# Performance work log

Measured on AMD Instinct MI355X. Metric: run time of the kernel, lower is better.

Reference implementation:

```python
import jax, jax.numpy as jnp
import numpy as np

N_SRC = 100000
N_DST = 50000
N_EDGES = 800000
D = 128
D_OUT = 128


def setup_inputs() -> dict:
    key = jax.random.key(0)
    ks = jax.random.split(key, 8)
    H_src = jax.random.normal(ks[0], (N_SRC, D), dtype=jnp.float32)
    H_dst = jax.random.normal(ks[1], (N_DST, D), dtype=jnp.float32)
    HBar_src = jax.random.normal(ks[2], (N_SRC, D), dtype=jnp.float32)
    agg_HBar_dst = jax.random.normal(ks[3], (N_DST, D), dtype=jnp.float32)
    src_idx = jax.random.randint(ks[4], (N_EDGES,), 0, N_SRC, dtype=jnp.int64)
    dst_idx = jax.random.randint(ks[5], (N_EDGES,), 0, N_DST, dtype=jnp.int64)
    # Linear(in_feats*2, out_feats): store as [2D, D_OUT] for x @ W + b
    gain = float(np.sqrt(2.0))  # calculate_gain('relu')
    bound = gain * float(np.sqrt(6.0 / (2 * D + D_OUT)))  # xavier_uniform
    W = jax.random.uniform(ks[6], (2 * D, D_OUT), dtype=jnp.float32,
                           minval=-bound, maxval=bound)
    b = jnp.zeros((D_OUT,), dtype=jnp.float32)
    return {"H_src": H_src, "H_dst": H_dst, "HBar_src": HBar_src,
            "agg_HBar_dst": agg_HBar_dst, "W": W, "b": b,
            "src_idx": src_idx, "dst_idx": dst_idx}


def reference(H_src, H_dst, HBar_src, agg_HBar_dst, W, b, src_idx, dst_idx):
    # training path of SAGEConvWithCV: copy_u('hdelta') + mean over dst
    hdelta = H_src - HBar_src                      # [N_src, D]
    msgs = jnp.take(hdelta, src_idx, axis=0)       # [E, D] gather
    summed = jax.ops.segment_sum(msgs, dst_idx, num_segments=N_DST)  # [N_dst, D]
    deg = jax.ops.segment_sum(jnp.ones((src_idx.shape[0],), dtype=H_src.dtype),
                              dst_idx, num_segments=N_DST)           # [N_dst]
    hdelta_new = summed / jnp.maximum(deg, 1.0)[:, None]  # mean (0 for isolated)
    h_neigh = agg_HBar_dst + hdelta_new
    h = jnp.concatenate([H_dst, h_neigh], axis=1) @ W + b  # [N_dst, D_OUT]
    return jax.nn.relu(h)
```

## Files before the change

kernel.cpp:

```cpp
#include <hip/hip_runtime.h>
#include <hip/hip_bf16.h>
#include <cstdint>
#include <cstddef>

#define NSRC 100000
#define NDST 50000
#define DOUT 128
#define KK2 256
#define NBUCK 196
#define CHUNK 4096

typedef __attribute__((ext_vector_type(8))) short bf16x8;
typedef __attribute__((ext_vector_type(4))) float f32x4;
typedef __attribute__((ext_vector_type(2))) float f32x2;

static __device__ __forceinline__ unsigned short f2bf(float f) {
    union { float f; uint32_t u; } v; v.f = f;
    uint32_t u = v.u;
    uint32_t r = u + 0x7FFFu + ((u >> 16) & 1u);
    return (unsigned short)(r >> 16);
}

__global__ __launch_bounds__(256) void k_prep(const float* __restrict__ W,
                                              unsigned short* __restrict__ WT,
                                              int* __restrict__ bcnt) {
    int i = blockIdx.x * 256 + threadIdx.x;
    if (i < DOUT * KK2) {
        int n = i >> 8;
        int k = i & 255;
        WT[i] = f2bf(W[k * DOUT + n]);
    }
    if (i < 256) bcnt[i] = 0;
}

__global__ __launch_bounds__(256) void k_hdelta(const float4* __restrict__ a,
                                                const float4* __restrict__ b,
                                                uint2* __restrict__ o, int n8) {
    int i = blockIdx.x * 256 + threadIdx.x;
    if (i < n8) {
        float4 x0 = a[i * 2],     y0 = b[i * 2];
        float4 x1 = a[i * 2 + 1], y1 = b[i * 2 + 1];
        uint32_t p0 = __builtin_amdgcn_cvt_pk_fp8_f32(x0.x - y0.x, x0.y - y0.y, 0u, false);
        p0 = __builtin_amdgcn_cvt_pk_fp8_f32(x0.z - y0.z, x0.w - y0.w, p0, true);
        uint32_t p1 = __builtin_amdgcn_cvt_pk_fp8_f32(x1.x - y1.x, x1.y - y1.y, 0u, false);
        p1 = __builtin_amdgcn_cvt_pk_fp8_f32(x1.z - y1.z, x1.w - y1.w, p1, true);
        o[i] = make_uint2(p0, p1);
    }
}

__global__ __launch_bounds__(256) void k_binA1(const int* __restrict__ dst,
                                               int* __restrict__ bcnt, int E) {
    __shared__ int bh[NBUCK];
    int t = threadIdx.x;
    if (t < NBUCK) bh[t] = 0;
    __syncthreads();
    int base = blockIdx.x * CHUNK;
    for (int i = t; i < CHUNK; i += 256) {
        int e = base + i;
        if (e < E) atomicAdd(&bh[dst[e] >> 8], 1);
    }
    __syncthreads();
    if (t < NBUCK && bh[t]) atomicAdd(&bcnt[t], bh[t]);
}

__global__ __launch_bounds__(256) void k_scanB(const int* __restrict__ bcnt,
                                               int* __restrict__ bbase,
                                               int* __restrict__ bcur,
                                               int* __restrict__ off, int E) {
    int t = threadIdx.x;
    int v = (t < NBUCK) ? bcnt[t] : 0;
    int lane = t & 63, w = t >> 6;
    int x = v;
#pragma unroll
    for (int s = 1; s < 64; s <<= 1) { int tt = __shfl_up(x, s, 64); if (lane >= s) x += tt; }
    __shared__ int wsum[4], wex[4];
    if (lane == 63) wsum[w] = x;
    __syncthreads();
    if (t == 0) {
        int run = 0;
#pragma unroll
        for (int k = 0; k < 4; ++k) { wex[k] = run; run += wsum[k]; }
    }
    __syncthreads();
    int ex = wex[w] + x - v;
    if (t < NBUCK) { bbase[t] = ex; bcur[t] = ex; }
    if (t == 0) off[NDST] = E;
}

__global__ __launch_bounds__(256) void k_binA2(const int* __restrict__ src,
                                               const int* __restrict__ dst,
                                               int* __restrict__ bcur,
                                               uint32_t* __restrict__ pairs, int E) {
    __shared__ int bh[NBUCK];
    __shared__ int lcur[NBUCK];
    int t = threadIdx.x;
    if (t < NBUCK) bh[t] = 0;
    __syncthreads();
    int base = blockIdx.x * CHUNK;
    for (int i = t; i < CHUNK; i += 256) {
        int e = base + i;
        if (e < E) atomicAdd(&bh[dst[e] >> 8], 1);
    }
    __syncthreads();
    if (t < NBUCK) lcur[t] = bh[t] ? atomicAdd(&bcur[t], bh[t]) : 0;
    __syncthreads();
    for (int i = t; i < CHUNK; i += 256) {
        int e = base + i;
        if (e < E) {
            int d = dst[e];
            int pos = atomicAdd(&lcur[d >> 8], 1);
            pairs[pos] = ((uint32_t)(d & 255) << 24) | (uint32_t)src[e];
        }
    }
}

__global__ __launch_bounds__(256) void k_binB(const uint32_t* __restrict__ pairs,
                                              const int* __restrict__ bcnt,
                                              const int* __restrict__ bbase,
                                              int* __restrict__ off,
                                              int* __restrict__ idx) {
    __shared__ int lcnt[256];
    __shared__ int lcur[256];
    __shared__ int wsum[4], wex[4];
    int b = blockIdx.x, t = threadIdx.x;
    int cnt = bcnt[b], gbase = bbase[b];
    lcnt[t] = 0;
    __syncthreads();
    for (int i = t; i < cnt; i += 256)
        atomicAdd(&lcnt[pairs[gbase + i] >> 24], 1);
    __syncthreads();
    int v = lcnt[t];
    int lane = t & 63, w = t >> 6;
    int x = v;
#pragma unroll
    for (int s = 1; s < 64; s <<= 1) { int tt = __shfl_up(x, s, 64); if (lane >= s) x += tt; }
    if (lane == 63) wsum[w] = x;
    __syncthreads();
    if (t == 0) {
        int run = 0;
#pragma unroll
        for (int k = 0; k < 4; ++k) { wex[k] = run; run += wsum[k]; }
    }
    __syncthreads();
    int ex = wex[w] + x - v;
    lcur[t] = ex;
    int d = b * 256 + t;
    if (d < NDST) off[d] = gbase + ex;
    __syncthreads();
    for (int i = t; i < cnt; i += 256) {
        uint32_t p = pairs[gbase + i];
        int pos = atomicAdd(&lcur[p >> 24], 1);
        idx[gbase + pos] = (int)(p & 0xFFFFFFu);
    }
}

__global__ __launch_bounds__(256) void k_gath(const unsigned short* __restrict__ hd8,
                                              const float2* __restrict__ agg,
                                              const int* __restrict__ off,
                                              const int* __restrict__ idx,
                                              ushort2* __restrict__ Xn, int n) {
    int r = blockIdx.x * 4 + (threadIdx.x >> 6);
    if (r >= n) return;
    int lane = threadIdx.x & 63;
    int o0 = off[r], o1 = off[r + 1];
    float accx = 0.f, accy = 0.f;
    for (int c = o0; c < o1; c += 64) {
        int m = o1 - c; if (m > 64) m = 64;
        int myi = (lane < m) ? idx[c + lane] : 0;
        int jm = m & ~7;
        for (int j = 0; j < jm; j += 8) {
            int s0 = __shfl(myi, j + 0), s1 = __shfl(myi, j + 1);
            int s2 = __shfl(myi, j + 2), s3 = __shfl(myi, j + 3);
            int s4 = __shfl(myi, j + 4), s5 = __shfl(myi, j + 5);
            int s6 = __shfl(myi, j + 6), s7 = __shfl(myi, j + 7);
            unsigned int u0 = hd8[(size_t)s0 * 64 + lane];
            unsigned int u1 = hd8[(size_t)s1 * 64 + lane];
            unsigned int u2 = hd8[(size_t)s2 * 64 + lane];
            unsigned int u3 = hd8[(size_t)s3 * 64 + lane];
            unsigned int u4 = hd8[(size_t)s4 * 64 + lane];
            unsigned int u5 = hd8[(size_t)s5 * 64 + lane];
            unsigned int u6 = hd8[(size_t)s6 * 64 + lane];
            unsigned int u7 = hd8[(size_t)s7 * 64 + lane];
            f32x2 d0 = __builtin_amdgcn_cvt_pk_f32_fp8(u0, false);
            f32x2 d1 = __builtin_amdgcn_cvt_pk_f32_fp8(u1, false);
            f32x2 d2 = __builtin_amdgcn_cvt_pk_f32_fp8(u2, false);
            f32x2 d3 = __builtin_amdgcn_cvt_pk_f32_fp8(u3, false);
            f32x2 d4 = __builtin_amdgcn_cvt_pk_f32_fp8(u4, false);
            f32x2 d5 = __builtin_amdgcn_cvt_pk_f32_fp8(u5, false);
            f32x2 d6 = __builtin_amdgcn_cvt_pk_f32_fp8(u6, false);
            f32x2 d7 = __builtin_amdgcn_cvt_pk_f32_fp8(u7, false);
            accx += d0[0] + d1[0] + d2[0] + d3[0] + d4[0] + d5[0] + d6[0] + d7[0];
            accy += d0[1] + d1[1] + d2[1] + d3[1] + d4[1] + d5[1] + d6[1] + d7[1];
        }
        for (int j = jm; j < m; ++j) {
            int s = __shfl(myi, j);
            unsigned int u = hd8[(size_t)s * 64 + lane];
            f32x2 d = __builtin_amdgcn_cvt_pk_f32_fp8(u, false);
            accx += d[0];
            accy += d[1];
        }
    }
    float inv = 1.0f / fmaxf((float)(o1 - o0), 1.0f);
    float2 g = agg[(size_t)r * 64 + lane];
    Xn[(size_t)r * 64 + lane] = make_ushort2(f2bf(g.x + accx * inv),
                                             f2bf(g.y + accy * inv));
}

__global__ __launch_bounds__(256) void k_gemm(const float4* __restrict__ Hd4,
                                              const unsigned short* __restrict__ Xn,
                                              const unsigned short* __restrict__ WT,
                                              const float* __restrict__ bias,
                                              float* __restrict__ out) {
    __shared__ __align__(16) unsigned short xt[16][264];
    int r0 = blockIdx.x * 16;
    int t = threadIdx.x;

    {
        int row = t >> 4, col8 = (t & 15) * 8;
        const float4* hrow = Hd4 + (size_t)(r0 + row) * 32 + (col8 >> 2);
        float4 p = hrow[0], q = hrow[1];
        bf16x8 hv;
        hv[0] = (short)f2bf(p.x); hv[1] = (short)f2bf(p.y);
        hv[2] = (short)f2bf(p.z); hv[3] = (short)f2bf(p.w);
        hv[4] = (short)f2bf(q.x); hv[5] = (short)f2bf(q.y);
        hv[6] = (short)f2bf(q.z); hv[7] = (short)f2bf(q.w);
        *(bf16x8*)&xt[row][col8] = hv;
        bf16x8 xv = *reinterpret_cast<const bf16x8*>(Xn + (size_t)(r0 + row) * 128 + col8);
        *(bf16x8*)&xt[row][128 + col8] = xv;
    }
    __syncthreads();

    int w = t >> 6, lane = t & 63;
    int lr = lane & 15, lg = lane >> 4;
    const bf16x8* B0 = reinterpret_cast<const bf16x8*>(WT + (size_t)(w * 32 + lr) * KK2 + lg * 8);
    const bf16x8* B1 = reinterpret_cast<const bf16x8*>(WT + (size_t)(w * 32 + 16 + lr) * KK2 + lg * 8);

    f32x4 acc0 = {0.f, 0.f, 0.f, 0.f};
    f32x4 acc1 = {0.f, 0.f, 0.f, 0.f};
#pragma unroll
    for (int kk = 0; kk < 8; ++kk) {
        bf16x8 av = *reinterpret_cast<const bf16x8*>(&xt[lr][lg * 8 + kk * 32]);
        acc0 = __builtin_amdgcn_mfma_f32_16x16x32_bf16(av, B0[kk * 4], acc0, 0, 0, 0);
        acc1 = __builtin_amdgcn_mfma_f32_16x16x32_bf16(av, B1[kk * 4], acc1, 0, 0, 0);
    }

    int col0 = w * 32 + lr;
    int col1 = col0 + 16;
    float bi0 = bias[col0], bi1 = bias[col1];
    int rowb = r0 + lg * 4;
#pragma unroll
    for (int j = 0; j < 4; ++j) {
        float v0 = acc0[j] + bi0;
        float v1 = acc1[j] + bi1;
        out[(size_t)(rowb + j) * DOUT + col0] = v0 > 0.f ? v0 : 0.f;
        out[(size_t)(rowb + j) * DOUT + col1] = v1 > 0.f ? v1 : 0.f;
    }
}

extern "C" void kernel_launch(void* const* d_in, const int* in_sizes, int n_in,
                              void* d_out, int out_size, void* d_ws, size_t ws_size,
                              hipStream_t stream) {
    const float* H_src    = (const float*)d_in[0];
    const float* H_dst    = (const float*)d_in[1];
    const float* HBar_src = (const float*)d_in[2];
    const float* agg      = (const float*)d_in[3];
    const float* W        = (const float*)d_in[4];
    const float* bias     = (const float*)d_in[5];
    const int*   src      = (const int*)d_in[6];
    const int*   dst      = (const int*)d_in[7];
    float* out = (float*)d_out;
    const int E = in_sizes[6];

    char* ws = (char*)d_ws;
    int* bcnt            = (int*)ws;
    int* bbase           = (int*)(ws + 1024);
    int* bcur            = (int*)(ws + 2048);
    int* off             = (int*)(ws + 3072);
    uint32_t* pairs      = (uint32_t*)(ws + 203264);
    int* idx_sorted      = (int*)(ws + 3403264);
    unsigned short* WT   = (unsigned short*)(ws + 6603264);
    unsigned short* hd8  = (unsigned short*)(ws + 6668800);
    unsigned short* Xn   = (unsigned short*)(ws + 19468800);

    const int NBE = (E + CHUNK - 1) / CHUNK;

    k_prep<<<128, 256, 0, stream>>>(W, WT, bcnt);

    int n8 = NSRC * 16;
    k_hdelta<<<(n8 + 255) / 256, 256, 0, stream>>>(
        (const float4*)H_src, (const float4*)HBar_src, (uint2*)hd8, n8);

    k_binA1<<<NBE, 256, 0, stream>>>(dst, bcnt, E);
    k_scanB<<<1, 256, 0, stream>>>(bcnt, bbase, bcur, off, E);
    k_binA2<<<NBE, 256, 0, stream>>>(src, dst, bcur, pairs, E);
    k_binB<<<NBUCK, 256, 0, stream>>>(pairs, bcnt, bbase, off, idx_sorted);

    k_gath<<<(NDST + 3) / 4, 256, 0, stream>>>(
        hd8, (const float2*)agg, off, idx_sorted, (ushort2*)Xn, NDST);

    k_gemm<<<NDST / 16, 256, 0, stream>>>(
        (const float4*)H_dst, Xn, WT, bias, out);
}
```

Baseline: 126.6 us.

## Fuse hdelta with bucket count, fold scan into binning, widen gather loads

Result: faster. 119.4 us (-5.7%).

```diff
diff --git a/kernel.cpp b/kernel.cpp
--- a/kernel.cpp
+++ b/kernel.cpp
@@ -23,35 +23,59 @@
 
 __global__ __launch_bounds__(256) void k_prep(const float* __restrict__ W,
                                               unsigned short* __restrict__ WT,
-                                              int* __restrict__ bcnt) {
+                                              int* __restrict__ bcnt,
+                                              int* __restrict__ bcur2) {
     int i = blockIdx.x * 256 + threadIdx.x;
     if (i < DOUT * KK2) {
         int n = i >> 8;
         int k = i & 255;
         WT[i] = f2bf(W[k * DOUT + n]);
     }
-    if (i < 256) bcnt[i] = 0;
-}
-
-__global__ __launch_bounds__(256) void k_hdelta(const float4* __restrict__ a,
-                                                const float4* __restrict__ b,
-                                                uint2* __restrict__ o, int n8) {
-    int i = blockIdx.x * 256 + threadIdx.x;
-    if (i < n8) {
-        float4 x0 = a[i * 2],     y0 = b[i * 2];
-        float4 x1 = a[i * 2 + 1], y1 = b[i * 2 + 1];
-        uint32_t p0 = __builtin_amdgcn_cvt_pk_fp8_f32(x0.x - y0.x, x0.y - y0.y, 0u, false);
-        p0 = __builtin_amdgcn_cvt_pk_fp8_f32(x0.z - y0.z, x0.w - y0.w, p0, true);
-        uint32_t p1 = __builtin_amdgcn_cvt_pk_fp8_f32(x1.x - y1.x, x1.y - y1.y, 0u, false);
-        p1 = __builtin_amdgcn_cvt_pk_fp8_f32(x1.z - y1.z, x1.w - y1.w, p1, true);
-        o[i] = make_uint2(p0, p1);
-    }
-}
-
-__global__ __launch_bounds__(256) void k_binA1(const int* __restrict__ dst,
-                                               int* __restrict__ bcnt, int E) {
+    if (i < 256) { bcnt[i] = 0; bcur2[i] = 0; }
+}
+
+__global__ __launch_bounds__(256) void k_hd_binA1(const float4* __restrict__ a,
+                                                  const float4* __restrict__ b,
+                                                  uint2* __restrict__ o, int n8,
+                                                  const int* __restrict__ dst,
+                                                  int* __restrict__ bcnt,
+                                                  int E, int nbe) {
     __shared__ int bh[NBUCK];
     int t = threadIdx.x;
+    if ((int)blockIdx.x < nbe) {
+        if (t < NBUCK) bh[t] = 0;
+        __syncthreads();
+        int base = blockIdx.x * CHUNK;
+        for (int i = t; i < CHUNK; i += 256) {
+            int e = base + i;
+            if (e < E) atomicAdd(&bh[dst[e] >> 8], 1);
+        }
+        __syncthreads();
+        if (t < NBUCK && bh[t]) atomicAdd(&bcnt[t], bh[t]);
+    } else {
+        int i = ((int)blockIdx.x - nbe) * 256 + t;
+        if (i < n8) {
+            float4 x0 = a[i * 2],     y0 = b[i * 2];
+            float4 x1 = a[i * 2 + 1], y1 = b[i * 2 + 1];
+            uint32_t p0 = __builtin_amdgcn_cvt_pk_fp8_f32(x0.x - y0.x, x0.y - y0.y, 0u, false);
+            p0 = __builtin_amdgcn_cvt_pk_fp8_f32(x0.z - y0.z, x0.w - y0.w, p0, true);
+            uint32_t p1 = __builtin_amdgcn_cvt_pk_fp8_f32(x1.x - y1.x, x1.y - y1.y, 0u, false);
+            p1 = __builtin_amdgcn_cvt_pk_fp8_f32(x1.z - y1.z, x1.w - y1.w, p1, true);
+            o[i] = make_uint2(p0, p1);
+        }
+    }
+}
+
+__global__ __launch_bounds__(256) void k_binA2(const int* __restrict__ src,
+                                               const int* __restrict__ dst,
+                                               const int* __restrict__ bcnt,
+                                               int* __restrict__ bcur2,
+                                               uint32_t* __restrict__ pairs, int E) {
+    __shared__ int bh[NBUCK], lcur[NBUCK];
+    __shared__ int wsum[4], wex[4];
+    int t = threadIdx.x;
+    int lane = t & 63, w = t >> 6;
+
     if (t < NBUCK) bh[t] = 0;
     __syncthreads();
     int base = blockIdx.x * CHUNK;
@@ -59,21 +83,11 @@
         int e = base + i;
         if (e < E) atomicAdd(&bh[dst[e] >> 8], 1);
     }
-    __syncthreads();
-    if (t < NBUCK && bh[t]) atomicAdd(&bcnt[t], bh[t]);
-}
-
-__global__ __launch_bounds__(256) void k_scanB(const int* __restrict__ bcnt,
-                                               int* __restrict__ bbase,
-                                               int* __restrict__ bcur,
-                                               int* __restrict__ off, int E) {
-    int t = threadIdx.x;
+
     int v = (t < NBUCK) ? bcnt[t] : 0;
-    int lane = t & 63, w = t >> 6;
     int x = v;
 #pragma unroll
     for (int s = 1; s < 64; s <<= 1) { int tt = __shfl_up(x, s, 64); if (lane >= s) x += tt; }
-    __shared__ int wsum[4], wex[4];
     if (lane == 63) wsum[w] = x;
     __syncthreads();
     if (t == 0) {
@@ -83,27 +97,10 @@
     }
     __syncthreads();
     int ex = wex[w] + x - v;
-    if (t < NBUCK) { bbase[t] = ex; bcur[t] = ex; }
-    if (t == 0) off[NDST] = E;
-}
-
-__global__ __launch_bounds__(256) void k_binA2(const int* __restrict__ src,
-                                               const int* __restrict__ dst,
-                                               int* __restrict__ bcur,
-                                               uint32_t* __restrict__ pairs, int E) {
-    __shared__ int bh[NBUCK];
-    __shared__ int lcur[NBUCK];
-    int t = threadIdx.x;
-    if (t < NBUCK) bh[t] = 0;
-    __syncthreads();
-    int base = blockIdx.x * CHUNK;
-    for (int i = t; i < CHUNK; i += 256) {
-        int e = base + i;
-        if (e < E) atomicAdd(&bh[dst[e] >> 8], 1);
-    }
-    __syncthreads();
-    if (t < NBUCK) lcur[t] = bh[t] ? atomicAdd(&bcur[t], bh[t]) : 0;
-    __syncthreads();
+
+    if (t < NBUCK) lcur[t] = bh[t] ? (ex + atomicAdd(&bcur2[t], bh[t])) : 0;
+    __syncthreads();
+
     for (int i = t; i < CHUNK; i += 256) {
         int e = base + i;
         if (e < E) {
@@ -116,22 +113,39 @@
 
 __global__ __launch_bounds__(256) void k_binB(const uint32_t* __restrict__ pairs,
                                               const int* __restrict__ bcnt,
-                                              const int* __restrict__ bbase,
                                               int* __restrict__ off,
-                                              int* __restrict__ idx) {
+                                              int* __restrict__ idx, int E) {
     __shared__ int lcnt[256];
     __shared__ int lcur[256];
     __shared__ int wsum[4], wex[4];
+    __shared__ int gbase_s;
     int b = blockIdx.x, t = threadIdx.x;
-    int cnt = bcnt[b], gbase = bbase[b];
+    int lane = t & 63, w = t >> 6;
+
+    int v = (t < NBUCK) ? bcnt[t] : 0;
+    int x = v;
+#pragma unroll
+    for (int s = 1; s < 64; s <<= 1) { int tt = __shfl_up(x, s, 64); if (lane >= s) x += tt; }
+    if (lane == 63) wsum[w] = x;
+    __syncthreads();
+    if (t == 0) {
+        int run = 0;
+#pragma unroll
+        for (int k = 0; k < 4; ++k) { wex[k] = run; run += wsum[k]; }
+    }
+    __syncthreads();
+    if (t == b) gbase_s = wex[w] + x - v;
     lcnt[t] = 0;
     __syncthreads();
+    int gbase = gbase_s;
+    int cnt = bcnt[b];
+
     for (int i = t; i < cnt; i += 256)
         atomicAdd(&lcnt[pairs[gbase + i] >> 24], 1);
     __syncthreads();
-    int v = lcnt[t];
-    int lane = t & 63, w = t >> 6;
-    int x = v;
+
+    v = lcnt[t];
+    x = v;
 #pragma unroll
     for (int s = 1; s < 64; s <<= 1) { int tt = __shfl_up(x, s, 64); if (lane >= s) x += tt; }
     if (lane == 63) wsum[w] = x;
@@ -146,7 +160,9 @@
     lcur[t] = ex;
     int d = b * 256 + t;
     if (d < NDST) off[d] = gbase + ex;
-    __syncthreads();
+    if (b == 0 && t == 0) off[NDST] = E;
+    __syncthreads();
+
     for (int i = t; i < cnt; i += 256) {
         uint32_t p = pairs[gbase + i];
         int pos = atomicAdd(&lcur[p >> 24], 1);
@@ -154,56 +170,79 @@
     }
 }
 
-__global__ __launch_bounds__(256) void k_gath(const unsigned short* __restrict__ hd8,
-                                              const float2* __restrict__ agg,
+__global__ __launch_bounds__(256) void k_gath(const uint32_t* __restrict__ hd8u,
+                                              const float4* __restrict__ agg4,
                                               const int* __restrict__ off,
                                               const int* __restrict__ idx,
-                                              ushort2* __restrict__ Xn, int n) {
+                                              ushort4* __restrict__ Xn, int n) {
     int r = blockIdx.x * 4 + (threadIdx.x >> 6);
     if (r >= n) return;
     int lane = threadIdx.x & 63;
+    int li = lane & 31, half = lane >> 5;
+    float a0 = 0.f, a1 = 0.f, a2 = 0.f, a3 = 0.f;
     int o0 = off[r], o1 = off[r + 1];
-    float accx = 0.f, accy = 0.f;
     for (int c = o0; c < o1; c += 64) {
         int m = o1 - c; if (m > 64) m = 64;
         int myi = (lane < m) ? idx[c + lane] : 0;
-        int jm = m & ~7;
-        for (int j = 0; j < jm; j += 8) {
-            int s0 = __shfl(myi, j + 0), s1 = __shfl(myi, j + 1);
-            int s2 = __shfl(myi, j + 2), s3 = __shfl(myi, j + 3);
-            int s4 = __shfl(myi, j + 4), s5 = __shfl(myi, j + 5);
-            int s6 = __shfl(myi, j + 6), s7 = __shfl(myi, j + 7);
-            unsigned int u0 = hd8[(size_t)s0 * 64 + lane];
-            unsigned int u1 = hd8[(size_t)s1 * 64 + lane];
-            unsigned int u2 = hd8[(size_t)s2 * 64 + lane];
-            unsigned int u3 = hd8[(size_t)s3 * 64 + lane];
-            unsigned int u4 = hd8[(size_t)s4 * 64 + lane];
-            unsigned int u5 = hd8[(size_t)s5 * 64 + lane];
-            unsigned int u6 = hd8[(size_t)s6 * 64 + lane];
-            unsigned int u7 = hd8[(size_t)s7 * 64 + lane];
-            f32x2 d0 = __builtin_amdgcn_cvt_pk_f32_fp8(u0, false);
-            f32x2 d1 = __builtin_amdgcn_cvt_pk_f32_fp8(u1, false);
-            f32x2 d2 = __builtin_amdgcn_cvt_pk_f32_fp8(u2, false);
-            f32x2 d3 = __builtin_amdgcn_cvt_pk_f32_fp8(u3, false);
-            f32x2 d4 = __builtin_amdgcn_cvt_pk_f32_fp8(u4, false);
-            f32x2 d5 = __builtin_amdgcn_cvt_pk_f32_fp8(u5, false);
-            f32x2 d6 = __builtin_amdgcn_cvt_pk_f32_fp8(u6, false);
-            f32x2 d7 = __builtin_amdgcn_cvt_pk_f32_fp8(u7, false);
-            accx += d0[0] + d1[0] + d2[0] + d3[0] + d4[0] + d5[0] + d6[0] + d7[0];
-            accy += d0[1] + d1[1] + d2[1] + d3[1] + d4[1] + d5[1] + d6[1] + d7[1];
-        }
-        for (int j = jm; j < m; ++j) {
-            int s = __shfl(myi, j);
-            unsigned int u = hd8[(size_t)s * 64 + lane];
-            f32x2 d = __builtin_amdgcn_cvt_pk_f32_fp8(u, false);
-            accx += d[0];
-            accy += d[1];
-        }
-    }
-    float inv = 1.0f / fmaxf((float)(o1 - o0), 1.0f);
-    float2 g = agg[(size_t)r * 64 + lane];
-    Xn[(size_t)r * 64 + lane] = make_ushort2(f2bf(g.x + accx * inv),
-                                             f2bf(g.y + accy * inv));
+        int j = 0;
+        for (; j + 16 <= m; j += 16) {
+            int s0 = __shfl(myi, j + 0 + half);
+            int s1 = __shfl(myi, j + 2 + half);
+            int s2 = __shfl(myi, j + 4 + half);
+            int s3 = __shfl(myi, j + 6 + half);
+            int s4 = __shfl(myi, j + 8 + half);
+            int s5 = __shfl(myi, j + 10 + half);
+            int s6 = __shfl(myi, j + 12 + half);
+            int s7 = __shfl(myi, j + 14 + half);
+            uint32_t u0 = hd8u[(size_t)s0 * 32 + li];
+            uint32_t u1 = hd8u[(size_t)s1 * 32 + li];
+            uint32_t u2 = hd8u[(size_t)s2 * 32 + li];
+            uint32_t u3 = hd8u[(size_t)s3 * 32 + li];
+            uint32_t u4 = hd8u[(size_t)s4 * 32 + li];
+            uint32_t u5 = hd8u[(size_t)s5 * 32 + li];
+            uint32_t u6 = hd8u[(size_t)s6 * 32 + li];
+            uint32_t u7 = hd8u[(size_t)s7 * 32 + li];
+            f32x2 l0 = __builtin_amdgcn_cvt_pk_f32_fp8(u0, false);
+            f32x2 h0 = __builtin_amdgcn_cvt_pk_f32_fp8(u0, true);
+            f32x2 l1 = __builtin_amdgcn_cvt_pk_f32_fp8(u1, false);
+            f32x2 h1 = __builtin_amdgcn_cvt_pk_f32_fp8(u1, true);
+            f32x2 l2 = __builtin_amdgcn_cvt_pk_f32_fp8(u2, false);
+            f32x2 h2 = __builtin_amdgcn_cvt_pk_f32_fp8(u2, true);
+            f32x2 l3 = __builtin_amdgcn_cvt_pk_f32_fp8(u3, false);
+            f32x2 h3 = __builtin_amdgcn_cvt_pk_f32_fp8(u3, true);
+            f32x2 l4 = __builtin_amdgcn_cvt_pk_f32_fp8(u4, false);
+            f32x2 h4 = __builtin_amdgcn_cvt_pk_f32_fp8(u4, true);
+            f32x2 l5 = __builtin_amdgcn_cvt_pk_f32_fp8(u5, false);
+            f32x2 h5 = __builtin_amdgcn_cvt_pk_f32_fp8(u5, true);
+            f32x2 l6 = __builtin_amdgcn_cvt_pk_f32_fp8(u6, false);
+            f32x2 h6 = __builtin_amdgcn_cvt_pk_f32_fp8(u6, true);
+            f32x2 l7 = __builtin_amdgcn_cvt_pk_f32_fp8(u7, false);
+            f32x2 h7 = __builtin_amdgcn_cvt_pk_f32_fp8(u7, true);
+            a0 += l0[0] + l1[0] + l2[0] + l3[0] + l4[0] + l5[0] + l6[0] + l7[0];
+            a1 += l0[1] + l1[1] + l2[1] + l3[1] + l4[1] + l5[1] + l6[1] + l7[1];
+            a2 += h0[0] + h1[0] + h2[0] + h3[0] + h4[0] + h5[0] + h6[0] + h7[0];
+            a3 += h0[1] + h1[1] + h2[1] + h3[1] + h4[1] + h5[1] + h6[1] + h7[1];
+        }
+        for (; j < m; j += 2) {
+            int tt = j + half;
+            int s = __shfl(myi, (tt < m) ? tt : 0);
+            uint32_t u = hd8u[(size_t)s * 32 + li];
+            if (tt >= m) u = 0;
+            f32x2 lo = __builtin_amdgcn_cvt_pk_f32_fp8(u, false);
+            f32x2 hi = __builtin_amdgcn_cvt_pk_f32_fp8(u, true);
+            a0 += lo[0]; a1 += lo[1]; a2 += hi[0]; a3 += hi[1];
+        }
+    }
+    a0 += __shfl_xor(a0, 32); a1 += __shfl_xor(a1, 32);
+    a2 += __shfl_xor(a2, 32); a3 += __shfl_xor(a3, 32);
+    if (half == 0) {
+        float inv = 1.0f / fmaxf((float)(o1 - o0), 1.0f);
+        float4 g = agg4[(size_t)r * 32 + li];
+        ushort4 u;
+        u.x = f2bf(g.x + a0 * inv); u.y = f2bf(g.y + a1 * inv);
+        u.z = f2bf(g.z + a2 * inv); u.w = f2bf(g.w + a3 * inv);
+        Xn[(size_t)r * 32 + li] = u;
+    }
 }
 
 __global__ __launch_bounds__(256) void k_gemm(const float4* __restrict__ Hd4,
@@ -273,8 +312,7 @@
 
     char* ws = (char*)d_ws;
     int* bcnt            = (int*)ws;
-    int* bbase           = (int*)(ws + 1024);
-    int* bcur            = (int*)(ws + 2048);
+    int* bcur2           = (int*)(ws + 1024);
     int* off             = (int*)(ws + 3072);
     uint32_t* pairs      = (uint32_t*)(ws + 203264);
     int* idx_sorted      = (int*)(ws + 3403264);
@@ -283,20 +321,21 @@
     unsigned short* Xn   = (unsigned short*)(ws + 19468800);
 
     const int NBE = (E + CHUNK - 1) / CHUNK;
-
-    k_prep<<<128, 256, 0, stream>>>(W, WT, bcnt);
-
     int n8 = NSRC * 16;
-    k_hdelta<<<(n8 + 255) / 256, 256, 0, stream>>>(
-        (const float4*)H_src, (const float4*)HBar_src, (uint2*)hd8, n8);
-
-    k_binA1<<<NBE, 256, 0, stream>>>(dst, bcnt, E);
-    k_scanB<<<1, 256, 0, stream>>>(bcnt, bbase, bcur, off, E);
-    k_binA2<<<NBE, 256, 0, stream>>>(src, dst, bcur, pairs, E);
-    k_binB<<<NBUCK, 256, 0, stream>>>(pairs, bcnt, bbase, off, idx_sorted);
+    int nStream = (n8 + 255) / 256;
+
+    k_prep<<<128, 256, 0, stream>>>(W, WT, bcnt, bcur2);
+
+    k_hd_binA1<<<NBE + nStream, 256, 0, stream>>>(
+        (const float4*)H_src, (const float4*)HBar_src, (uint2*)hd8, n8,
+        dst, bcnt, E, NBE);
+
+    k_binA2<<<NBE, 256, 0, stream>>>(src, dst, bcnt, bcur2, pairs, E);
+    k_binB<<<NBUCK, 256, 0, stream>>>(pairs, bcnt, off, idx_sorted, E);
 
     k_gath<<<(NDST + 3) / 4, 256, 0, stream>>>(
-        hd8, (const float2*)agg, off, idx_sorted, (ushort2*)Xn, NDST);
+        (const uint32_t*)hd8, (const float4*)agg, off, idx_sorted,
+        (ushort4*)Xn, NDST);
 
     k_gemm<<<NDST / 16, 256, 0, stream>>>(
         (const float4*)H_dst, Xn, WT, bias, out);
```
